# Kernel tuning notes

Measured on AMD Instinct MI355X. Metric: run time of the kernel, lower is better.

The kernel has to match this reference:

```python
import jax, jax.numpy as jnp
import numpy as np

N_NODES = 50000
N_EDGES = 800000
IN_CH, OUT_CH, HEADS = 64, 32, 4
NEG_SLOPE = 0.2
BN_EPS = 1e-5


def setup_inputs() -> dict:
    key = jax.random.key(0)
    ks = jax.random.split(key, 9)
    x = jax.random.normal(ks[0], (N_NODES, IN_CH), dtype=jnp.float32)
    pos = jax.random.uniform(ks[1], (N_NODES, 3), dtype=jnp.float32)
    edge_index = jax.random.randint(ks[2], (2, N_EDGES), 0, N_NODES, dtype=jnp.int64)
    s = 1.0 / np.sqrt(IN_CH)
    W_l = jax.random.normal(ks[3], (IN_CH, HEADS * OUT_CH), dtype=jnp.float32) * s
    W_r = jax.random.normal(ks[4], (IN_CH, HEADS * OUT_CH), dtype=jnp.float32) * s
    W_edge = jax.random.normal(ks[5], (3, HEADS * OUT_CH), dtype=jnp.float32) * 0.5
    att = jax.random.normal(ks[6], (HEADS, OUT_CH), dtype=jnp.float32) * (1.0 / np.sqrt(OUT_CH))
    bn_gamma = jax.random.uniform(ks[7], (HEADS * OUT_CH,), dtype=jnp.float32, minval=0.5, maxval=1.5)
    bn_beta = jax.random.normal(ks[8], (HEADS * OUT_CH,), dtype=jnp.float32) * 0.1
    return {"x": x, "pos": pos, "edge_index": edge_index, "W_l": W_l, "W_r": W_r,
            "W_edge": W_edge, "att": att, "bn_gamma": bn_gamma, "bn_beta": bn_beta}


def reference(x, pos, edge_index, W_l, W_r, W_edge, att, bn_gamma, bn_beta):
    N = x.shape[0]
    H, C = att.shape
    # source->target projections (GATv2: lin_l for source/messages, lin_r for target)
    xl = (x @ W_l).reshape(N, H, C)
    xr = (x @ W_r).reshape(N, H, C)
    src, dst = edge_index[0], edge_index[1]
    edge_attr = pos[src] - pos[dst]  # [E,3] relative position as edge feature
    # add self-loops with fill_value='mean' (PyG default)
    loop = jnp.arange(N)
    src = jnp.concatenate([src, loop])
    dst = jnp.concatenate([dst, loop])
    mean_attr = edge_attr.mean(axis=0, keepdims=True)  # [1,3]
    edge_attr = jnp.concatenate([edge_attr, jnp.broadcast_to(mean_attr, (N, 3))], axis=0)
    # per-edge GATv2 score: att . LeakyReLU(x_l[j] + x_r[i] + W_e e_ij)
    e_feat = (edge_attr @ W_edge).reshape(-1, H, C)
    msg = xl[src]                              # [Et,H,C] (reused for aggregation)
    e = msg + xr[dst] + e_feat
    e = jax.nn.leaky_relu(e, NEG_SLOPE)
    score = jnp.einsum('ehc,hc->eh', e, att)   # [Et,H]
    # segment softmax over destination node
    m = jax.ops.segment_max(score, dst, num_segments=N)
    score = jnp.exp(score - m[dst])
    denom = jax.ops.segment_sum(score, dst, num_segments=N)
    alpha = score / (denom[dst] + 1e-16)       # [Et,H]
    out = jax.ops.segment_sum(alpha[:, :, None] * msg, dst, num_segments=N)
    out = out.reshape(N, H * C)
    # BatchNorm over node dimension (training-mode batch statistics, PyG BatchNorm)
    mu = out.mean(axis=0)
    var = out.var(axis=0)
    return (out - mu) / jnp.sqrt(var + BN_EPS) * bn_gamma + bn_beta
```

## Files before the change

### kernel.cpp

```cpp
#include <hip/hip_runtime.h>
#include <hip/hip_bf16.h>

#define N_NODES 50000
#define IN_CH 64
#define HC 128
#define CAP 64
#define NEG_SLOPE 0.2f
#define BN_EPS 1e-5f

#define BIN_SH 7
#define BIN_N  128
#define NBINS  391
#define BINCAP 8192


__global__ __launch_bounds__(256) void k_bin(const int* __restrict__ eidx,
                                             unsigned int* __restrict__ binbuf,
                                             int* __restrict__ bin_count,
                                             int E) {
  __shared__ int hist[NBINS];
  __shared__ int base_l[NBINS];
  __shared__ int s_w64;

  if (threadIdx.x < 64) {
    int w = eidx[2 * threadIdx.x + 1];
    unsigned long long nz = __ballot(w != 0);
    if (threadIdx.x == 0) s_w64 = (nz == 0ULL) ? 1 : 0;
  }
  for (int b = threadIdx.x; b < NBINS; b += 256) hist[b] = 0;
  __syncthreads();
  const bool w64 = s_w64 != 0;

  const int tid = blockIdx.x * 256 + threadIdx.x;
  const int base = tid * 8;
  const bool vec_ok = w64 ? ((E & 1) == 0) : ((E & 3) == 0);

  int s[8], d[8];
  int n = 0;
  if (base + 8 <= E && vec_ok) {
    if (w64) {
      const int4* ps = (const int4*)(eidx + 2 * base);
      int4 A = ps[0], B = ps[1], C = ps[2], D = ps[3];
      s[0]=A.x; s[1]=A.z; s[2]=B.x; s[3]=B.z; s[4]=C.x; s[5]=C.z; s[6]=D.x; s[7]=D.z;
      const int4* pd = (const int4*)(eidx + 2 * E + 2 * base);
      A = pd[0]; B = pd[1]; C = pd[2]; D = pd[3];
      d[0]=A.x; d[1]=A.z; d[2]=B.x; d[3]=B.z; d[4]=C.x; d[5]=C.z; d[6]=D.x; d[7]=D.z;
    } else {
      int4 A = *(const int4*)(eidx + base);
      int4 B = *(const int4*)(eidx + base + 4);
      s[0]=A.x; s[1]=A.y; s[2]=A.z; s[3]=A.w; s[4]=B.x; s[5]=B.y; s[6]=B.z; s[7]=B.w;
      A = *(const int4*)(eidx + E + base);
      B = *(const int4*)(eidx + E + base + 4);
      d[0]=A.x; d[1]=A.y; d[2]=A.z; d[3]=A.w; d[4]=B.x; d[5]=B.y; d[6]=B.z; d[7]=B.w;
    }
    n = 8;
  } else if (base < E) {
    int hi = min(base + 8, E);
    for (int e = base; e < hi; ++e) {
      if (w64) { s[n] = eidx[2 * e]; d[n] = eidx[2 * (E + e)]; }
      else     { s[n] = eidx[e];     d[n] = eidx[E + e]; }
      ++n;
    }
  }

  int bin[8], rank[8];
  for (int k = 0; k < n; ++k) {
    bin[k] = d[k] >> BIN_SH;
    rank[k] = atomicAdd(&hist[bin[k]], 1);
  }
  __syncthreads();
  for (int b = threadIdx.x; b < NBINS; b += 256) {
    int h = hist[b];
    base_l[b] = h ? atomicAdd(&bin_count[b], h) : 0;
  }
  __syncthreads();
  for (int k = 0; k < n; ++k) {
    int idx = base_l[bin[k]] + rank[k];
    if (idx < BINCAP)
      binbuf[bin[k] * BINCAP + idx] = ((unsigned int)(d[k] & (BIN_N - 1)) << 16) | (unsigned int)s[k];
  }
}

__global__ __launch_bounds__(256) void k_bucket(const unsigned int* __restrict__ binbuf,
                                                const int* __restrict__ bin_count,
                                                const float* __restrict__ pos,
                                                int* __restrict__ deg,
                                                int* __restrict__ srcs,
                                                float* __restrict__ mean_sums) {
  __shared__ unsigned int srcs_l[BIN_N * CAP];
  __shared__ int deg_l[BIN_N];
  __shared__ float red[4][3];

  const int bin = blockIdx.x;
  const int nbase = bin << BIN_SH;
  const int nn = min(BIN_N, N_NODES - nbase);

  if (threadIdx.x < BIN_N) deg_l[threadIdx.x] = 1;
  __syncthreads();

  const int cnt = min(bin_count[bin], BINCAP);
  float sx = 0.f, sy = 0.f, sz = 0.f;

  for (int t = threadIdx.x; t < cnt; t += 256) {
    unsigned int rec = binbuf[bin * BINCAP + t];
    int s  = (int)(rec & 0xffffu);
    int dl = (int)((rec >> 16) & 0xffu);
    int slot = atomicAdd(&deg_l[dl], 1);
    if (slot < CAP) srcs_l[(dl << 6) + slot] = (unsigned int)s;
    int dg = nbase + dl;
    sx += pos[3 * s]     - pos[3 * dg];
    sy += pos[3 * s + 1] - pos[3 * dg + 1];
    sz += pos[3 * s + 2] - pos[3 * dg + 2];
  }

  #pragma unroll
  for (int m = 1; m < 64; m <<= 1) {
    sx += __shfl_xor(sx, m); sy += __shfl_xor(sy, m); sz += __shfl_xor(sz, m);
  }
  int wave = threadIdx.x >> 6, lane = threadIdx.x & 63;
  if (lane == 0) { red[wave][0] = sx; red[wave][1] = sy; red[wave][2] = sz; }
  __syncthreads();
  if (threadIdx.x == 0) {
    float a = 0.f, b = 0.f, c = 0.f;
    for (int w = 0; w < 4; ++w) { a += red[w][0]; b += red[w][1]; c += red[w][2]; }
    unsafeAtomicAdd(&mean_sums[0], a);
    unsafeAtomicAdd(&mean_sums[1], b);
    unsafeAtomicAdd(&mean_sums[2], c);
  }

  if (threadIdx.x < nn) deg[nbase + threadIdx.x] = deg_l[threadIdx.x];
  const int nw4 = nn << 4;
  uint4* dstp = (uint4*)(srcs + (size_t)nbase * CAP);
  const uint4* srcp = (const uint4*)srcs_l;
  for (int t = threadIdx.x; t < nw4; t += 256) dstp[t] = srcp[t];
}

__global__ __launch_bounds__(256) void k_gemm(const float* __restrict__ x,
                                              const float* __restrict__ Wl,
                                              const float* __restrict__ Wr,
                                              unsigned int* __restrict__ xl_bf,
                                              float* __restrict__ xr_out) {
  __shared__ float xs[16][IN_CH];
  __shared__ __hip_bfloat162 wsm[IN_CH][128];
  const int t = threadIdx.x;
  const int row0 = blockIdx.x * 16;

  for (int i = 0; i < 32; ++i) {
    int k = i * 2 + (t >> 7);
    int p = t & 127;
    int cc = p * 2;
    float2 wv;
    if (cc < 128) wv = *(const float2*)(Wl + k * 128 + cc);
    else          wv = *(const float2*)(Wr + k * 128 + (cc - 128));
    wsm[k][p] = __float22bfloat162_rn(wv);
  }
  {
    int r = t >> 4, c4 = (t & 15) * 4;
    *(float4*)&xs[r][c4] = *(const float4*)(x + (row0 + r) * IN_CH + c4);
  }
  __syncthreads();

  const int ct = t & 63;
  const int rt = t >> 6;
  const int c4 = ct * 4;
  const int r4 = rt * 4;

  float acc[4][4];
  #pragma unroll
  for (int a = 0; a < 4; ++a)
    #pragma unroll
    for (int b = 0; b < 4; ++b) acc[a][b] = 0.f;

  #pragma unroll 8
  for (int k = 0; k < IN_CH; ++k) {
    uint2 wraw = *(const uint2*)&wsm[k][ct * 2];
    float2 f01 = __bfloat1622float2(*(__hip_bfloat162*)&wraw.x);
    float2 f23 = __bfloat1622float2(*(__hip_bfloat162*)&wraw.y);
    float wv[4] = {f01.x, f01.y, f23.x, f23.y};
    float xv[4] = {xs[r4][k], xs[r4 + 1][k], xs[r4 + 2][k], xs[r4 + 3][k]};
    #pragma unroll
    for (int a = 0; a < 4; ++a)
      #pragma unroll
      for (int b = 0; b < 4; ++b) acc[a][b] = fmaf(xv[a], wv[b], acc[a][b]);
  }

  #pragma unroll
  for (int a = 0; a < 4; ++a) {
    int row = row0 + r4 + a;
    if (c4 < 128) {
      __hip_bfloat162 b01 = __float22bfloat162_rn(make_float2(acc[a][0], acc[a][1]));
      __hip_bfloat162 b23 = __float22bfloat162_rn(make_float2(acc[a][2], acc[a][3]));
      uint2 u;
      u.x = *(unsigned int*)&b01;
      u.y = *(unsigned int*)&b23;
      *(uint2*)(xl_bf + row * 64 + (c4 >> 1)) = u;
    } else {
      float4 v = make_float4(acc[a][0], acc[a][1], acc[a][2], acc[a][3]);
      *(float4*)(xr_out + row * HC + (c4 - 128)) = v;
    }
  }
}

__device__ __forceinline__ float sum8_dpp(float v) {
  v += __int_as_float(__builtin_amdgcn_mov_dpp(__float_as_int(v), 0xB1,  0xF, 0xF, true));
  v += __int_as_float(__builtin_amdgcn_mov_dpp(__float_as_int(v), 0x4E,  0xF, 0xF, true));
  v += __int_as_float(__builtin_amdgcn_mov_dpp(__float_as_int(v), 0x141, 0xF, 0xF, true));
  return v;
}

__device__ __forceinline__ void edge4(int s, float dx, float dy, float dz, bool valid,
                                      const unsigned int* __restrict__ xl_bf, int l5,
                                      float4 xr4, float4 at4, float4 w0, float4 w1, float4 w2,
                                      float& a0, float& a1, float& a2, float& a3, float& den) {
  uint2 raw = *(const uint2*)(xl_bf + (s << 6) + (l5 << 1));
  float2 x01 = __bfloat1622float2(*(__hip_bfloat162*)&raw.x);
  float2 x23 = __bfloat1622float2(*(__hip_bfloat162*)&raw.y);
  float t0 = x01.x + xr4.x; t0 = fmaf(dx, w0.x, t0); t0 = fmaf(dy, w1.x, t0); t0 = fmaf(dz, w2.x, t0);
  float t1 = x01.y + xr4.y; t1 = fmaf(dx, w0.y, t1); t1 = fmaf(dy, w1.y, t1); t1 = fmaf(dz, w2.y, t1);
  float t2 = x23.x + xr4.z; t2 = fmaf(dx, w0.z, t2); t2 = fmaf(dy, w1.z, t2); t2 = fmaf(dz, w2.z, t2);
  float t3 = x23.y + xr4.w; t3 = fmaf(dx, w0.w, t3); t3 = fmaf(dy, w1.w, t3); t3 = fmaf(dz, w2.w, t3);
  float l0 = fmaxf(t0, NEG_SLOPE * t0);
  float l1 = fmaxf(t1, NEG_SLOPE * t1);
  float l2 = fmaxf(t2, NEG_SLOPE * t2);
  float l3 = fmaxf(t3, NEG_SLOPE * t3);
  float sc = l0 * at4.x;
  sc = fmaf(l1, at4.y, sc); sc = fmaf(l2, at4.z, sc); sc = fmaf(l3, at4.w, sc);
  sc = sum8_dpp(sc);
  float e = __expf(sc);
  float p = valid ? e : 0.f;
  den += p;
  a0 = fmaf(p, x01.x, a0); a1 = fmaf(p, x01.y, a1);
  a2 = fmaf(p, x23.x, a2); a3 = fmaf(p, x23.y, a3);
}

__global__ __launch_bounds__(256) void k_agg(const unsigned int* __restrict__ xl_bf,
                                             float* __restrict__ xr_out,
                                             const float* __restrict__ pos,
                                             const float* __restrict__ att,
                                             const float* __restrict__ We,
                                             const float* __restrict__ mean_sums,
                                             const int* __restrict__ srcs,
                                             const int* __restrict__ deg,
                                             float invE,
                                             float* __restrict__ bn_sums) {
  __shared__ __align__(16) float redS[4][128];
  __shared__ __align__(16) float redQ[4][128];
  const int lane = threadIdx.x & 63;
  const int half = lane >> 5;
  const int l5 = lane & 31;
  const int c = l5 << 2;
  const int wave = threadIdx.x >> 6;

  const float4 at4 = *(const float4*)(att + c);
  const float4 w0 = *(const float4*)(We + c);
  const float4 w1 = *(const float4*)(We + 128 + c);
  const float4 w2 = *(const float4*)(We + 256 + c);
  const float m0 = mean_sums[0] * invE;
  const float m1 = mean_sums[1] * invE;
  const float m2 = mean_sums[2] * invE;

  const int gw = blockIdx.x * 4 + wave;
  const int W = gridDim.x * 4;

  float4 bs = make_float4(0.f, 0.f, 0.f, 0.f);
  float4 bq = make_float4(0.f, 0.f, 0.f, 0.f);

  for (int i = gw; i < N_NODES; i += W) {
    const float4 xr4 = *(const float4*)(xr_out + i * HC + c);
    const float px = pos[3 * i], py = pos[3 * i + 1], pz = pos[3 * i + 2];
    const int di = min(deg[i], CAP);
    const int sreg = srcs[i * CAP + lane];
    float a0 = 0.f, a1 = 0.f, a2 = 0.f, a3 = 0.f, den = 0.f;

    {
      int sA = __shfl(sreg, 1);
      if (half == 0) sA = i;
      bool vA = half < di;
      if (!vA) sA = i;
      int jB = 2 + half;
      int sB = __shfl(sreg, jB);
      bool vB = jB < di;
      if (!vB) sB = i;
      float pax = pos[3 * sA], pay = pos[3 * sA + 1], paz = pos[3 * sA + 2];
      float pbx = pos[3 * sB], pby = pos[3 * sB + 1], pbz = pos[3 * sB + 2];
      float dxA = (half == 0) ? m0 : pax - px;
      float dyA = (half == 0) ? m1 : pay - py;
      float dzA = (half == 0) ? m2 : paz - pz;
      edge4(sA, dxA, dyA, dzA, vA, xl_bf, l5, xr4, at4, w0, w1, w2, a0, a1, a2, a3, den);
      edge4(sB, pbx - px, pby - py, pbz - pz, vB, xl_bf, l5, xr4, at4, w0, w1, w2, a0, a1, a2, a3, den);
    }

    for (int j = 4; j < di; j += 4) {
      int jA = j + half;
      int jB = j + 2 + half;
      int sA = __shfl(sreg, jA);
      int sB = __shfl(sreg, jB);
      bool vA = jA < di;
      bool vB = jB < di;
      if (!vA) sA = i;
      if (!vB) sB = i;
      float pax = pos[3 * sA], pay = pos[3 * sA + 1], paz = pos[3 * sA + 2];
      float pbx = pos[3 * sB], pby = pos[3 * sB + 1], pbz = pos[3 * sB + 2];
      edge4(sA, pax - px, pay - py, paz - pz, vA, xl_bf, l5, xr4, at4, w0, w1, w2, a0, a1, a2, a3, den);
      edge4(sB, pbx - px, pby - py, pbz - pz, vB, xl_bf, l5, xr4, at4, w0, w1, w2, a0, a1, a2, a3, den);
    }

    den += __shfl_xor(den, 32);
    a0 += __shfl_xor(a0, 32);
    a1 += __shfl_xor(a1, 32);
    a2 += __shfl_xor(a2, 32);
    a3 += __shfl_xor(a3, 32);

    const float inv = 1.f / (den + 1e-16f);
    if (half == 0) {
      float4 o = make_float4(a0 * inv, a1 * inv, a2 * inv, a3 * inv);
      *(float4*)(xr_out + i * HC + c) = o;
      bs.x += o.x; bs.y += o.y; bs.z += o.z; bs.w += o.w;
      bq.x = fmaf(o.x, o.x, bq.x); bq.y = fmaf(o.y, o.y, bq.y);
      bq.z = fmaf(o.z, o.z, bq.z); bq.w = fmaf(o.w, o.w, bq.w);
    }
  }

  if (half == 0) {
    *(float4*)&redS[wave][c] = bs;
    *(float4*)&redQ[wave][c] = bq;
  }
  __syncthreads();
  const int t = threadIdx.x;
  if (t < 128) {
    float s = redS[0][t] + redS[1][t] + redS[2][t] + redS[3][t];
    float q = redQ[0][t] + redQ[1][t] + redQ[2][t] + redQ[3][t];
    unsafeAtomicAdd(&bn_sums[t], s);
    unsafeAtomicAdd(&bn_sums[128 + t], q);
  }
}

__global__ __launch_bounds__(256) void k_bnapply(float* __restrict__ out,
                                                 const float* __restrict__ bn_sums,
                                                 const float* __restrict__ gamma,
                                                 const float* __restrict__ beta,
                                                 int n4) {
  const int stride = gridDim.x * blockDim.x;
  const float invN = 1.f / (float)N_NODES;
  for (int i = blockIdx.x * blockDim.x + threadIdx.x; i < n4; i += stride) {
    int c = (i & 31) * 4;
    float4 v = ((float4*)out)[i];
    float4 s = *(const float4*)(bn_sums + c);
    float4 q = *(const float4*)(bn_sums + 128 + c);
    float4 g = *(const float4*)(gamma + c);
    float4 b = *(const float4*)(beta + c);
    float mu, var, rstd;
    mu = s.x * invN; var = q.x * invN - mu * mu; rstd = rsqrtf(var + BN_EPS);
    v.x = (v.x - mu) * rstd * g.x + b.x;
    mu = s.y * invN; var = q.y * invN - mu * mu; rstd = rsqrtf(var + BN_EPS);
    v.y = (v.y - mu) * rstd * g.y + b.y;
    mu = s.z * invN; var = q.z * invN - mu * mu; rstd = rsqrtf(var + BN_EPS);
    v.z = (v.z - mu) * rstd * g.z + b.z;
    mu = s.w * invN; var = q.w * invN - mu * mu; rstd = rsqrtf(var + BN_EPS);
    v.w = (v.w - mu) * rstd * g.w + b.w;
    ((float4*)out)[i] = v;
  }
}

extern "C" void kernel_launch(void* const* d_in, const int* in_sizes, int n_in,
                              void* d_out, int out_size, void* d_ws, size_t ws_size,
                              hipStream_t stream) {
  const float* x     = (const float*)d_in[0];
  const float* pos   = (const float*)d_in[1];
  const int*   eidx  = (const int*)d_in[2];
  const float* Wl    = (const float*)d_in[3];
  const float* Wr    = (const float*)d_in[4];
  const float* We    = (const float*)d_in[5];
  const float* att   = (const float*)d_in[6];
  const float* gamma = (const float*)d_in[7];
  const float* beta  = (const float*)d_in[8];
  float* out = (float*)d_out;
  const int E = in_sizes[2] / 2;

  char* ws = (char*)d_ws;
  float* mean_sums     = (float*)(ws + 64);
  float* bn_sums       = (float*)(ws + 1024);
  int*   bin_count     = (int*)(ws + 4096);
  int*   deg           = (int*)(ws + 8192);
  int*   srcs          = (int*)(ws + 208896);
  unsigned int* binbuf = (unsigned int*)(ws + 13008896);
  unsigned int* xl_bf  = (unsigned int*)(ws + 25821184);

  hipMemsetAsync(ws, 0, 8192, stream);

  int bblocks = (E + 2047) / 2048;
  k_bin<<<bblocks, 256, 0, stream>>>(eidx, binbuf, bin_count, E);
  k_bucket<<<NBINS, 256, 0, stream>>>(binbuf, bin_count, pos, deg, srcs, mean_sums);
  k_gemm<<<N_NODES / 16, 256, 0, stream>>>(x, Wl, Wr, xl_bf, out);
  k_agg<<<2048, 256, 0, stream>>>(xl_bf, out, pos, att, We, mean_sums, srcs, deg,
                                  1.f / (float)E, bn_sums);
  k_bnapply<<<512, 256, 0, stream>>>(out, bn_sums, gamma, beta, out_size / 4);
}
```

Measured before the change: 239.5 us.

## Halve bin size, factor dst-pos out of mean sum, transpose x tile in GEMM

Node bins shrink from 128 to 64 nodes, doubling the number of bin blocks. The edge-mean accumulation now sums only source positions per edge and subtracts degree times the destination position once per node, which removes per-edge destination loads. The GEMM stores the x tile transposed with padding so each k step reads one float4 instead of four scalar LDS loads. The DPP 8-lane reduction is replaced by __shfl_xor, which likely costs more per edge since it goes through ds_bpermute.

```diff
diff --git a/kernel.cpp b/kernel.cpp
--- a/kernel.cpp
+++ b/kernel.cpp
@@ -8,10 +8,10 @@
 #define NEG_SLOPE 0.2f
 #define BN_EPS 1e-5f
 
-#define BIN_SH 7
-#define BIN_N  128
-#define NBINS  391
-#define BINCAP 8192
+#define BIN_SH 6
+#define BIN_N  64
+#define NBINS  782
+#define BINCAP 4096
 
 
 __global__ __launch_bounds__(256) void k_bin(const int* __restrict__ eidx,
@@ -107,10 +107,18 @@
     int dl = (int)((rec >> 16) & 0xffu);
     int slot = atomicAdd(&deg_l[dl], 1);
     if (slot < CAP) srcs_l[(dl << 6) + slot] = (unsigned int)s;
-    int dg = nbase + dl;
-    sx += pos[3 * s]     - pos[3 * dg];
-    sy += pos[3 * s + 1] - pos[3 * dg + 1];
-    sz += pos[3 * s + 2] - pos[3 * dg + 2];
+    sx += pos[3 * s];
+    sy += pos[3 * s + 1];
+    sz += pos[3 * s + 2];
+  }
+  __syncthreads();
+
+  if (threadIdx.x < nn) {
+    float cdeg = (float)(deg_l[threadIdx.x] - 1);
+    int dg = nbase + threadIdx.x;
+    sx -= cdeg * pos[3 * dg];
+    sy -= cdeg * pos[3 * dg + 1];
+    sz -= cdeg * pos[3 * dg + 2];
   }
 
   #pragma unroll
@@ -140,7 +148,7 @@
                                               const float* __restrict__ Wr,
                                               unsigned int* __restrict__ xl_bf,
                                               float* __restrict__ xr_out) {
-  __shared__ float xs[16][IN_CH];
+  __shared__ float xsT[64][20];
   __shared__ __hip_bfloat162 wsm[IN_CH][128];
   const int t = threadIdx.x;
   const int row0 = blockIdx.x * 16;
@@ -155,8 +163,12 @@
     wsm[k][p] = __float22bfloat162_rn(wv);
   }
   {
-    int r = t >> 4, c4 = (t & 15) * 4;
-    *(float4*)&xs[r][c4] = *(const float4*)(x + (row0 + r) * IN_CH + c4);
+    int r = t & 15, c4 = (t >> 4) * 4;
+    float4 v = *(const float4*)(x + (row0 + r) * IN_CH + c4);
+    xsT[c4 + 0][r] = v.x;
+    xsT[c4 + 1][r] = v.y;
+    xsT[c4 + 2][r] = v.z;
+    xsT[c4 + 3][r] = v.w;
   }
   __syncthreads();
 
@@ -177,7 +189,8 @@
     float2 f01 = __bfloat1622float2(*(__hip_bfloat162*)&wraw.x);
     float2 f23 = __bfloat1622float2(*(__hip_bfloat162*)&wraw.y);
     float wv[4] = {f01.x, f01.y, f23.x, f23.y};
-    float xv[4] = {xs[r4][k], xs[r4 + 1][k], xs[r4 + 2][k], xs[r4 + 3][k]};
+    float4 xv4 = *(const float4*)&xsT[k][r4];
+    float xv[4] = {xv4.x, xv4.y, xv4.z, xv4.w};
     #pragma unroll
     for (int a = 0; a < 4; ++a)
       #pragma unroll
@@ -199,13 +212,6 @@
       *(float4*)(xr_out + row * HC + (c4 - 128)) = v;
     }
   }
-}
-
-__device__ __forceinline__ float sum8_dpp(float v) {
-  v += __int_as_float(__builtin_amdgcn_mov_dpp(__float_as_int(v), 0xB1,  0xF, 0xF, true));
-  v += __int_as_float(__builtin_amdgcn_mov_dpp(__float_as_int(v), 0x4E,  0xF, 0xF, true));
-  v += __int_as_float(__builtin_amdgcn_mov_dpp(__float_as_int(v), 0x141, 0xF, 0xF, true));
-  return v;
 }
 
 __device__ __forceinline__ void edge4(int s, float dx, float dy, float dz, bool valid,
@@ -225,7 +231,7 @@
   float l3 = fmaxf(t3, NEG_SLOPE * t3);
   float sc = l0 * at4.x;
   sc = fmaf(l1, at4.y, sc); sc = fmaf(l2, at4.z, sc); sc = fmaf(l3, at4.w, sc);
-  sc = sum8_dpp(sc);
+  sc += __shfl_xor(sc, 1); sc += __shfl_xor(sc, 2); sc += __shfl_xor(sc, 4);
   float e = __expf(sc);
   float p = valid ? e : 0.f;
   den += p;
```

Measured after the change: 260.4 us. 8.7% more time.
